# Kernel optimization log

Hardware: AMD Instinct MI355X
Metric: run time of the kernel (lower is better)

## Reference

```python
import jax, jax.numpy as jnp
import numpy as np

B, N, DIN, DOUT, EIN, EOUT = 8, 256, 64, 64, 64, 64


def setup_inputs() -> dict:
    key = jax.random.key(0)
    ks = jax.random.split(key, 9)
    A = jax.random.randint(ks[0], (B, N, N), 0, 2).astype(jnp.float32)  # {0,1} connectivity
    emb_node = jax.random.normal(ks[1], (B, N, DIN), dtype=jnp.float32)
    emb_edge = jax.random.normal(ks[2], (B, N, N, EIN), dtype=jnp.float32)
    s_n = 1.0 / np.sqrt(DIN)
    s_e = 1.0 / np.sqrt(EIN)
    Wn = jax.random.uniform(ks[3], (DIN, DOUT), minval=-s_n, maxval=s_n)
    bn = jax.random.uniform(ks[4], (DOUT,), minval=-s_n, maxval=s_n)
    Wsn = jax.random.uniform(ks[5], (DIN, DOUT), minval=-s_n, maxval=s_n)
    bsn = jax.random.uniform(ks[6], (DOUT,), minval=-s_n, maxval=s_n)
    We = jax.random.uniform(ks[7], (EIN, EOUT), minval=-s_e, maxval=s_e)
    be = jax.random.uniform(ks[8], (EOUT,), minval=-s_e, maxval=s_e)
    return {"A": A, "emb_node": emb_node, "emb_edge": emb_edge,
            "Wn": Wn, "bn": bn, "Wsn": Wsn, "bsn": bsn, "We": We, "be": be}


def reference(A, emb_node, emb_edge, Wn, bn, Wsn, bsn, We, be):
    # mode=1 (default) of ChannelIndependentConv
    node_x = emb_node @ Wn + bn          # [B,N,DOUT]
    node_sx = emb_node @ Wsn + bsn       # [B,N,DOUT]
    edge_x = emb_edge @ We + be          # [B,N,N,EOUT]
    # mask edges by connectivity, then channel-independent aggregation:
    # out[b,i,c] = sum_j A[b,i,j] * edge_x[b,i,j,c] * node_x[b,j,c]
    Ae = A[..., None] * edge_x           # [B,N,N,EOUT]
    agg = jnp.einsum('bijc,bjc->bic', Ae, node_x)  # [B,N,DOUT]
    node_out = jax.nn.relu(agg) + jax.nn.relu(node_sx)
    edge_out = jax.nn.relu(edge_x)
    return node_out, edge_out
```

## Files before the change

### kernel.cpp

```cpp
#include <hip/hip_runtime.h>

#define BN   2048
#define NN   256
#define CH   64

typedef __attribute__((ext_vector_type(8))) short short8;
typedef __attribute__((ext_vector_type(4))) float fv4;

static __device__ inline short f2bf(float f) {
  unsigned u = __float_as_uint(f);
  u += 0x7FFF + ((u >> 16) & 1);
  return (short)(u >> 16);
}

static __device__ inline short8 cvt_frag(fv4 a, fv4 b) {
  union { short8 s; unsigned u[4]; } r;
  asm("v_cvt_pk_bf16_f32 %0, %1, %2" : "=v"(r.u[0]) : "v"(a[0]), "v"(a[1]));
  asm("v_cvt_pk_bf16_f32 %0, %1, %2" : "=v"(r.u[1]) : "v"(a[2]), "v"(a[3]));
  asm("v_cvt_pk_bf16_f32 %0, %1, %2" : "=v"(r.u[2]) : "v"(b[0]), "v"(b[1]));
  asm("v_cvt_pk_bf16_f32 %0, %1, %2" : "=v"(r.u[3]) : "v"(b[2]), "v"(b[3]));
  return r.s;
}

__global__ __launch_bounds__(256) void node_kernel(
    const float* __restrict__ emb_node, const float* __restrict__ Wn,
    const float* __restrict__ bn, const float* __restrict__ Wsn,
    const float* __restrict__ bsn, float* __restrict__ node_x,
    float* __restrict__ rsx) {
  __shared__ float s_emb[4][CH];
  __shared__ float s_Wn[CH * CH];
  __shared__ float s_Ws[CH * CH];
  const int tid = threadIdx.x;
  const int r = tid >> 6;
  const int c = tid & 63;
  const int row = blockIdx.x * 4 + r;
#pragma unroll
  for (int i = 0; i < 4; ++i) {
    *(fv4*)&s_Wn[(i * 256 + tid) * 4] = *(const fv4*)&Wn[(i * 256 + tid) * 4];
    *(fv4*)&s_Ws[(i * 256 + tid) * 4] = *(const fv4*)&Wsn[(i * 256 + tid) * 4];
  }
  s_emb[r][c] = emb_node[row * CH + c];
  __syncthreads();
  float a1 = bn[c], a2 = bsn[c];
#pragma unroll
  for (int k = 0; k < CH; ++k) {
    const float e = s_emb[r][k];
    a1 = fmaf(e, s_Wn[k * CH + c], a1);
    a2 = fmaf(e, s_Ws[k * CH + c], a2);
  }
  node_x[row * CH + c] = a1;
  rsx[row * CH + c] = fmaxf(a2, 0.0f);
}

__global__ __launch_bounds__(256, 8) void edge_mfma_kernel(
    const float* __restrict__ A, const float* __restrict__ emb_edge,
    const float* __restrict__ We, const float* __restrict__ be,
    const float* __restrict__ node_x, const float* __restrict__ rsx,
    float* __restrict__ node_out, float* __restrict__ edge_out) {
  const int bi   = blockIdx.x;
  const int b    = bi >> 8;
  const int tid  = threadIdx.x;
  const int lane = tid & 63;
  const int wave = tid >> 6;
  const int l15  = lane & 15;
  const int quad = lane >> 4;
  const int c    = wave * 16 + l15;

  const float* __restrict__ ee = emb_edge + (size_t)bi * NN * CH;
  float*       __restrict__ eo = edge_out + (size_t)bi * NN * CH;
  const float* __restrict__ nx = node_x + (size_t)b * NN * CH;
  const float* __restrict__ Ar = A + (size_t)bi * NN;

  short8 bfrag[2];
#pragma unroll
  for (int h = 0; h < 2; ++h)
#pragma unroll
    for (int j = 0; j < 8; ++j)
      bfrag[h][j] = f2bf(We[(h * 32 + quad * 8 + j) * CH + c]);
  const float bias = be[c];

  float agg = 0.0f;

  for (int t = 0; t < 16; ++t) {
    const int j0 = t * 16;
    const float* rp = ee + (j0 + l15) * CH + quad * 8;
    const fv4 a0 = *(const fv4*)(rp);
    const fv4 a1 = *(const fv4*)(rp + 4);
    const fv4 a2 = *(const fv4*)(rp + 32);
    const fv4 a3 = *(const fv4*)(rp + 36);
    const fv4 av = *(const fv4*)(Ar + j0 + quad * 4);
    const int rb = j0 + quad * 4;
    float nxv[4];
#pragma unroll
    for (int r = 0; r < 4; ++r) nxv[r] = nx[(rb + r) * CH + c];

    const short8 af0 = cvt_frag(a0, a1);
    const short8 af1 = cvt_frag(a2, a3);
    fv4 acc = {bias, bias, bias, bias};
    acc = __builtin_amdgcn_mfma_f32_16x16x32_bf16(af0, bfrag[0], acc, 0, 0, 0);
    acc = __builtin_amdgcn_mfma_f32_16x16x32_bf16(af1, bfrag[1], acc, 0, 0, 0);
#pragma unroll
    for (int r = 0; r < 4; ++r) {
      const float ex = acc[r];
      __builtin_nontemporal_store(fmaxf(ex, 0.0f), eo + (rb + r) * CH + c);
      agg = fmaf(av[r] * ex, nxv[r], agg);
    }
  }

  agg += __shfl_xor(agg, 16, 64);
  agg += __shfl_xor(agg, 32, 64);
  if (quad == 0) {
    node_out[(size_t)bi * CH + c] =
        fmaxf(agg, 0.0f) + rsx[(size_t)bi * CH + c];
  }
}

extern "C" void kernel_launch(void* const* d_in, const int* in_sizes, int n_in,
                              void* d_out, int out_size, void* d_ws, size_t ws_size,
                              hipStream_t stream) {
  const float* A        = (const float*)d_in[0];
  const float* emb_node = (const float*)d_in[1];
  const float* emb_edge = (const float*)d_in[2];
  const float* Wn       = (const float*)d_in[3];
  const float* bn       = (const float*)d_in[4];
  const float* Wsn      = (const float*)d_in[5];
  const float* bsn      = (const float*)d_in[6];
  const float* We       = (const float*)d_in[7];
  const float* be       = (const float*)d_in[8];

  float* node_out = (float*)d_out;
  float* edge_out = (float*)d_out + (size_t)BN * CH;

  float* node_x = (float*)d_ws;
  float* rsx    = (float*)d_ws + (size_t)BN * CH;

  hipLaunchKernelGGL(node_kernel, dim3(BN / 4), dim3(256), 0, stream,
                     emb_node, Wn, bn, Wsn, bsn, node_x, rsx);
  hipLaunchKernelGGL(edge_mfma_kernel, dim3(BN), dim3(256), 0, stream,
                     A, emb_edge, We, be, node_x, rsx, node_out, edge_out);
}
```

Measured before the change: 291.3 us.

## Software-pipeline edge kernel loads with inline asm and transposed MFMA output

```diff
diff --git a/kernel.cpp b/kernel.cpp
--- a/kernel.cpp
+++ b/kernel.cpp
@@ -52,7 +52,7 @@
   rsx[row * CH + c] = fmaxf(a2, 0.0f);
 }
 
-__global__ __launch_bounds__(256, 8) void edge_mfma_kernel(
+__global__ __launch_bounds__(256, 4) void edge_mfma_kernel(
     const float* __restrict__ A, const float* __restrict__ emb_edge,
     const float* __restrict__ We, const float* __restrict__ be,
     const float* __restrict__ node_x, const float* __restrict__ rsx,
@@ -64,54 +64,115 @@
   const int wave = tid >> 6;
   const int l15  = lane & 15;
   const int quad = lane >> 4;
-  const int c    = wave * 16 + l15;
+  const int cq   = wave * 16 + quad * 4;
 
   const float* __restrict__ ee = emb_edge + (size_t)bi * NN * CH;
   float*       __restrict__ eo = edge_out + (size_t)bi * NN * CH;
-  const float* __restrict__ nx = node_x + (size_t)b * NN * CH;
+  const float* __restrict__ nxp = node_x + (size_t)b * NN * CH;
   const float* __restrict__ Ar = A + (size_t)bi * NN;
 
-  short8 bfrag[2];
+  short8 wfrag[2];
 #pragma unroll
   for (int h = 0; h < 2; ++h)
 #pragma unroll
     for (int j = 0; j < 8; ++j)
-      bfrag[h][j] = f2bf(We[(h * 32 + quad * 8 + j) * CH + c]);
-  const float bias = be[c];
-
-  float agg = 0.0f;
-
-  for (int t = 0; t < 16; ++t) {
-    const int j0 = t * 16;
-    const float* rp = ee + (j0 + l15) * CH + quad * 8;
-    const fv4 a0 = *(const fv4*)(rp);
-    const fv4 a1 = *(const fv4*)(rp + 4);
-    const fv4 a2 = *(const fv4*)(rp + 32);
-    const fv4 a3 = *(const fv4*)(rp + 36);
-    const fv4 av = *(const fv4*)(Ar + j0 + quad * 4);
-    const int rb = j0 + quad * 4;
-    float nxv[4];
-#pragma unroll
-    for (int r = 0; r < 4; ++r) nxv[r] = nx[(rb + r) * CH + c];
-
-    const short8 af0 = cvt_frag(a0, a1);
-    const short8 af1 = cvt_frag(a2, a3);
-    fv4 acc = {bias, bias, bias, bias};
-    acc = __builtin_amdgcn_mfma_f32_16x16x32_bf16(af0, bfrag[0], acc, 0, 0, 0);
-    acc = __builtin_amdgcn_mfma_f32_16x16x32_bf16(af1, bfrag[1], acc, 0, 0, 0);
-#pragma unroll
-    for (int r = 0; r < 4; ++r) {
-      const float ex = acc[r];
-      __builtin_nontemporal_store(fmaxf(ex, 0.0f), eo + (rb + r) * CH + c);
-      agg = fmaf(av[r] * ex, nxv[r], agg);
-    }
-  }
-
-  agg += __shfl_xor(agg, 16, 64);
-  agg += __shfl_xor(agg, 32, 64);
-  if (quad == 0) {
-    node_out[(size_t)bi * CH + c] =
-        fmaxf(agg, 0.0f) + rsx[(size_t)bi * CH + c];
+      wfrag[h][j] = f2bf(We[(h * 32 + quad * 8 + j) * CH + wave * 16 + l15]);
+  const fv4 biasv = *(const fv4*)&be[cq];
+
+  const int voe = l15 * 256 + quad * 32;
+  const int vno = l15 * 256 + wave * 64 + quad * 16;
+  const int voa = l15 * 4;
+
+  fv4 e0[4], e1[4], e2[4], e3[4], nv[4];
+  float av[4];
+  fv4 agg = {0.f, 0.f, 0.f, 0.f};
+
+#define LGRP(T, S)                                                             \
+  {                                                                            \
+    const int ve = voe + (T) * 4096;                                           \
+    asm volatile("global_load_dwordx4 %0, %1, %2"                              \
+                 : "=v"(e0[S]) : "v"(ve), "s"(ee));                            \
+    asm volatile("global_load_dwordx4 %0, %1, %2 offset:16"                    \
+                 : "=v"(e1[S]) : "v"(ve), "s"(ee));                            \
+    asm volatile("global_load_dwordx4 %0, %1, %2 offset:128"                   \
+                 : "=v"(e2[S]) : "v"(ve), "s"(ee));                            \
+    asm volatile("global_load_dwordx4 %0, %1, %2 offset:144"                   \
+                 : "=v"(e3[S]) : "v"(ve), "s"(ee));                            \
+    const int vn = vno + (T) * 4096;                                           \
+    asm volatile("global_load_dwordx4 %0, %1, %2"                              \
+                 : "=v"(nv[S]) : "v"(vn), "s"(nxp));                           \
+    const int va = voa + (T) * 64;                                             \
+    asm volatile("global_load_dword %0, %1, %2"                                \
+                 : "=v"(av[S]) : "v"(va), "s"(Ar));                            \
+  }
+
+#define WAITSB(N)                                                              \
+  do {                                                                         \
+    asm volatile("s_waitcnt vmcnt(" #N ")" ::: "memory");                      \
+    __builtin_amdgcn_sched_barrier(0);                                         \
+  } while (0)
+
+#define COMP(T, S)                                                             \
+  {                                                                            \
+    const short8 af0 = cvt_frag(e0[S], e1[S]);                                 \
+    const short8 af1 = cvt_frag(e2[S], e3[S]);                                 \
+    fv4 acc = biasv;                                         \
+    acc = __builtin_amdgcn_mfma_f32_16x16x32_bf16(wfrag[0], af0, acc, 0,0,0);  \
+    acc = __builtin_amdgcn_mfma_f32_16x16x32_bf16(wfrag[1], af1, acc, 0,0,0);  \
+    fv4 rl;                                                                    \
+    _Pragma("unroll") for (int r = 0; r < 4; ++r) {                            \
+      rl[r] = fmaxf(acc[r], 0.0f);                                             \
+      agg[r] = fmaf(av[S] * acc[r], nv[S][r], agg[r]);                         \
+    }                                                                          \
+    const int vo = vno + (T) * 4096;                                           \
+    asm volatile("global_store_dwordx4 %0, %1, %2"                             \
+                 :: "v"(vo), "v"(rl), "s"(eo));                                \
+  }
+
+#define ITER(T, S, N, PF)                                                      \
+  {                                                                            \
+    WAITSB(N);                                                                 \
+    COMP(T, S)                                                                 \
+    if (PF) LGRP((T) + 4, S)                                                   \
+  }
+
+  LGRP(0, 0) LGRP(1, 1) LGRP(2, 2) LGRP(3, 3)
+
+  ITER(0, 0, 18, 1)
+  ITER(1, 1, 19, 1)
+  ITER(2, 2, 20, 1)
+  ITER(3, 3, 21, 1)
+  ITER(4, 0, 21, 1)
+  ITER(5, 1, 21, 1)
+  ITER(6, 2, 21, 1)
+  ITER(7, 3, 21, 1)
+  ITER(8, 0, 21, 1)
+  ITER(9, 1, 21, 1)
+  ITER(10, 2, 21, 1)
+  ITER(11, 3, 21, 1)
+  ITER(12, 0, 21, 0)
+  ITER(13, 1, 15, 0)
+  ITER(14, 2, 9, 0)
+  ITER(15, 3, 3, 0)
+
+#undef ITER
+#undef COMP
+#undef WAITSB
+#undef LGRP
+
+#pragma unroll
+  for (int r = 0; r < 4; ++r) {
+    agg[r] += __shfl_xor(agg[r], 1, 64);
+    agg[r] += __shfl_xor(agg[r], 2, 64);
+    agg[r] += __shfl_xor(agg[r], 4, 64);
+    agg[r] += __shfl_xor(agg[r], 8, 64);
+  }
+  if (l15 == 0) {
+    const fv4 rs = *(const fv4*)&rsx[(size_t)bi * CH + cq];
+    fv4 out;
+#pragma unroll
+    for (int r = 0; r < 4; ++r) out[r] = fmaxf(agg[r], 0.0f) + rs[r];
+    *(fv4*)&node_out[(size_t)bi * CH + cq] = out;
   }
 }
 
```

Measured after the change: 278.6 us. 4.4% less time.
